# Kernel optimization log

Hardware: AMD Instinct MI355X
Metric: run time of the kernel (lower is better)

The kernel has to match this reference:

```python
import jax, jax.numpy as jnp
import numpy as np
import math

D_MODEL = 1024
N_HEADS = 16
HEAD_DIM = D_MODEL // N_HEADS
N_LEVELS = 4
B = 8
MAX_LEN = 1024
LN_EPS = 1e-5


def setup_inputs() -> dict:
    key = jax.random.key(0)
    ks = jax.random.split(key, 6)
    lengths = np.array([1024, 768, 512, 896, 640, 1024, 576, 704], dtype=np.int32)
    N = int(lengths.sum())  # 6144
    batch_offsets = jnp.asarray(np.concatenate([[0], np.cumsum(lengths)]).astype(np.int32))
    x = jax.random.normal(ks[0], (N, D_MODEL), jnp.float32)
    levels = jax.random.randint(ks[1], (N, 1), 0, N_LEVELS).astype(jnp.float32)
    coords = jax.random.uniform(ks[2], (N, 2), jnp.float32) * 64.0
    positions = jnp.concatenate([levels, coords], axis=-1)  # [N, 3] = (level, y, x)
    ln_gamma = jnp.ones((D_MODEL,), jnp.float32)
    ln_beta = jnp.zeros((D_MODEL,), jnp.float32)
    w_qkv = jax.random.normal(ks[3], (D_MODEL, 3 * D_MODEL), jnp.float32) / math.sqrt(D_MODEL)
    w_out = jax.random.normal(ks[4], (D_MODEL, D_MODEL), jnp.float32) / math.sqrt(D_MODEL)
    # learned per-level, per-head rotary frequencies for 2 spatial coords
    base = 10.0 ** (-2.0 * np.arange(HEAD_DIM // 2) / HEAD_DIM)  # rope_theta = 10.0
    rope_freqs = (jnp.asarray(base, jnp.float32)[None, None, :, None]
                  * (1.0 + 0.1 * jax.random.normal(ks[5], (N_LEVELS, N_HEADS, HEAD_DIM // 2, 2), jnp.float32)))
    return {"x": x, "positions": positions, "batch_offsets": batch_offsets,
            "ln_gamma": ln_gamma, "ln_beta": ln_beta, "w_qkv": w_qkv,
            "w_out": w_out, "rope_freqs": rope_freqs}


def _layernorm(x, g, b):
    mu = jnp.mean(x, axis=-1, keepdims=True)
    var = jnp.mean(jnp.square(x - mu), axis=-1, keepdims=True)
    return (x - mu) * jax.lax.rsqrt(var + LN_EPS) * g + b


def _forward(x, positions, batch_offsets, ln_gamma, ln_beta, w_qkv, w_out, rope_freqs):
    N = x.shape[0]
    residual = x
    h = _layernorm(x, ln_gamma, ln_beta)
    q, k, v = jnp.split(h @ w_qkv, 3, axis=-1)  # each [N, D]

    # ragged -> padded batch layout
    tok = jnp.arange(N)
    batch_ids = jnp.searchsorted(batch_offsets[1:], tok, side='right')  # [N]
    pos_in_seq = tok - batch_offsets[batch_ids]                         # [N]
    lengths = batch_offsets[1:] - batch_offsets[:-1]                    # [B]
    valid = jnp.arange(MAX_LEN)[None, :] < lengths[:, None]             # [B, L]

    def pad(t, fill=0.0):
        out = jnp.full((B, MAX_LEN) + t.shape[1:], fill, t.dtype)
        return out.at[batch_ids, pos_in_seq].set(t)

    qp = pad(q).reshape(B, MAX_LEN, N_HEADS, HEAD_DIM)
    kp = pad(k).reshape(B, MAX_LEN, N_HEADS, HEAD_DIM)
    vp = pad(v).reshape(B, MAX_LEN, N_HEADS, HEAD_DIM)
    posp = pad(positions, fill=1.0)  # padded positions filled with ones (as in torch code)

    # multilevel RoPE: per-level learned freqs over 2 spatial coords
    lvl = jnp.clip(posp[..., 0].astype(jnp.int32), 0, N_LEVELS - 1)  # [B, L]
    f = rope_freqs[lvl]                                              # [B, L, H, K, 2]
    ang = jnp.einsum('blhkc,blc->blhk', f, posp[..., 1:])            # [B, L, H, K]
    cos, sin = jnp.cos(ang), jnp.sin(ang)

    def rot(t):  # rotate consecutive pairs of head_dim
        t = t.reshape(B, MAX_LEN, N_HEADS, HEAD_DIM // 2, 2)
        a, b = t[..., 0], t[..., 1]
        return jnp.stack([a * cos - b * sin, a * sin + b * cos], axis=-1).reshape(
            B, MAX_LEN, N_HEADS, HEAD_DIM)

    qr, kr = rot(qp), rot(kp)

    # masked SDPA (padded keys excluded; padded query rows are dropped on un-pad)
    scale = 1.0 / math.sqrt(HEAD_DIM)
    scores = jnp.einsum('blhd,bmhd->bhlm', qr, kr) * scale
    scores = jnp.where(valid[:, None, None, :], scores, jnp.float32(-1e9))
    attn = jax.nn.softmax(scores, axis=-1)
    o = jnp.einsum('bhlm,bmhd->blhd', attn, vp).reshape(B, MAX_LEN, D_MODEL)

    o = o[batch_ids, pos_in_seq]  # back to packed [N, D]
    return o @ w_out + residual


def reference(x, positions, batch_offsets, ln_gamma, ln_beta, w_qkv, w_out, rope_freqs):
    return _forward(x, positions, batch_offsets, ln_gamma, ln_beta, w_qkv, w_out, rope_freqs)
```

## Files before the change

kernel.cpp:

```cpp
#include <hip/hip_runtime.h>


typedef float  f32x4  __attribute__((ext_vector_type(4)));
typedef __bf16 bf16x8 __attribute__((ext_vector_type(8)));
typedef __bf16 bf16x4 __attribute__((ext_vector_type(4)));
typedef short  s16x4  __attribute__((ext_vector_type(4)));
typedef short  s16x8  __attribute__((ext_vector_type(8)));
typedef unsigned short u16x4 __attribute__((ext_vector_type(4)));

typedef __attribute__((address_space(1))) void as1_void_t;
typedef __attribute__((address_space(3))) void as3_void_t;

static __device__ __forceinline__ unsigned short f2bf(float f) {
  unsigned int u = __float_as_uint(f);
  u += 0x7fffu + ((u >> 16) & 1u);
  return (unsigned short)(u >> 16);
}
static __device__ __forceinline__ float bf2f(unsigned short s) {
  return __uint_as_float(((unsigned int)s) << 16);
}

static __device__ __forceinline__ void gload_lds16(const void* g, void* l) {
  __builtin_amdgcn_global_load_lds((as1_void_t*)g, (as3_void_t*)l, 16, 0, 0);
}

static __device__ __forceinline__ f32x4 mfma32(bf16x8 a, bf16x8 b, f32x4 c) {
  return __builtin_amdgcn_mfma_f32_16x16x32_bf16(a, b, c, 0, 0, 0);
}
static __device__ __forceinline__ f32x4 mfma16(s16x4 a, s16x4 b, f32x4 c) {
  return __builtin_amdgcn_mfma_f32_16x16x16bf16_1k(a, b, c, 0, 0, 0);
}

__global__ __launch_bounds__(256) void ln_kernel(
    const float* __restrict__ x, const float* __restrict__ gamma,
    const float* __restrict__ beta, unsigned short* __restrict__ h, int Ntok) {
  int row  = blockIdx.x * 4 + (threadIdx.x >> 6);
  int lane = threadIdx.x & 63;
  const float* xr = x + (size_t)row * 1024;
  f32x4 v[4];
  float s = 0.f, ss = 0.f;
#pragma unroll
  for (int c = 0; c < 4; ++c) {
    v[c] = *(const f32x4*)(xr + c * 256 + lane * 4);
#pragma unroll
    for (int j = 0; j < 4; ++j) { s += v[c][j]; ss += v[c][j] * v[c][j]; }
  }
#pragma unroll
  for (int d = 1; d < 64; d <<= 1) {
    s  += __shfl_xor(s, d);
    ss += __shfl_xor(ss, d);
  }
  float mu  = s * (1.f / 1024.f);
  float var = ss * (1.f / 1024.f) - mu * mu;
  float inv = rsqrtf(var + 1e-5f);
#pragma unroll
  for (int c = 0; c < 4; ++c) {
    f32x4 gv = *(const f32x4*)(gamma + c * 256 + lane * 4);
    f32x4 bv = *(const f32x4*)(beta  + c * 256 + lane * 4);
    u16x4 hv;
#pragma unroll
    for (int j = 0; j < 4; ++j) hv[j] = f2bf((v[c][j] - mu) * inv * gv[j] + bv[j]);
    *(u16x4*)(h + (size_t)row * 1024 + c * 256 + lane * 4) = hv;
  }
}

__global__ __launch_bounds__(256) void transpose_bf16(
    const float* __restrict__ in, unsigned short* __restrict__ out, int R, int C) {
  __shared__ unsigned short tile[64][65];
  int c0 = blockIdx.x * 64, r0 = blockIdx.y * 64;
  int t = threadIdx.x;
  int tr = t >> 6, tc = t & 63;
#pragma unroll
  for (int i = 0; i < 16; ++i) {
    int rr = i * 4 + tr;
    tile[tc][rr] = f2bf(in[(size_t)(r0 + rr) * C + c0 + tc]);
  }
  __syncthreads();
#pragma unroll
  for (int i = 0; i < 16; ++i) {
    int cc = i * 4 + tr;
    out[(size_t)(c0 + cc) * R + r0 + tc] = tile[cc][tc];
  }
}

__global__ __launch_bounds__(256) void gemm_qkv(
    const unsigned short* __restrict__ A, const unsigned short* __restrict__ Bt,
    unsigned short* __restrict__ Cqkv, int M, int K) {
  __shared__ unsigned short Alds[128 * 32];
  __shared__ unsigned short Blds[128 * 32];
  int n0 = blockIdx.x * 128, m0 = blockIdx.y * 128;
  int t = threadIdx.x, lane = t & 63, wave = t >> 6;
  int wr = wave >> 1, wc = wave & 1;
  int r = lane & 15, g = lane >> 4;
  f32x4 acc[4][4] = {};

  int srow = lane >> 2;
  int scol = (lane & 3) * 8;

  for (int k0 = 0; k0 < K; k0 += 32) {
    __syncthreads();
#pragma unroll
    for (int c = 0; c < 2; ++c) {
      int seg = wave * 2 + c;
      gload_lds16(A  + (size_t)(m0 + seg * 16 + srow) * K + k0 + scol,
                  Alds + seg * 16 * 32);
      gload_lds16(Bt + (size_t)(n0 + seg * 16 + srow) * K + k0 + scol,
                  Blds + seg * 16 * 32);
    }
    __syncthreads();
    bf16x8 a[4], b[4];
#pragma unroll
    for (int m = 0; m < 4; ++m)
      a[m] = *(const bf16x8*)(Alds + (wr * 64 + m * 16 + r) * 32 + g * 8);
#pragma unroll
    for (int n = 0; n < 4; ++n)
      b[n] = *(const bf16x8*)(Blds + (wc * 64 + n * 16 + r) * 32 + g * 8);
#pragma unroll
    for (int m = 0; m < 4; ++m)
#pragma unroll
      for (int n = 0; n < 4; ++n)
        acc[m][n] = mfma32(a[m], b[n], acc[m][n]);
  }

#pragma unroll
  for (int mi = 0; mi < 4; ++mi) {
    int grow0 = m0 + wr * 64 + mi * 16 + g * 4;
#pragma unroll
    for (int ni = 0; ni < 4; ++ni) {
      int gcol = n0 + wc * 64 + ni * 16 + r;
      f32x4 v = acc[mi][ni];
#pragma unroll
      for (int e = 0; e < 4; ++e) {
        int which = gcol >> 10, rem = gcol & 1023, hh = rem >> 6, d = rem & 63;
        Cqkv[((size_t)(which * 16 + hh) * M + grow0 + e) * 64 + d] = f2bf(v[e]);
      }
    }
  }
}

__global__ __launch_bounds__(256) void gemm_n64(
    const unsigned short* __restrict__ A, const unsigned short* __restrict__ Bt,
    const float* __restrict__ residual, float* __restrict__ Cf,
    int M, int Ncols, int K) {
  __shared__ unsigned short Alds[128 * 32];
  __shared__ unsigned short Blds[64 * 32];
  int n0 = blockIdx.x * 64, m0 = blockIdx.y * 128;
  int t = threadIdx.x, lane = t & 63, wave = t >> 6;
  int wr = wave >> 1, wc = wave & 1;
  int r = lane & 15, g = lane >> 4;
  f32x4 acc[4][2] = {};

  int srow = lane >> 2;
  int scol = (lane & 3) * 8;

  for (int k0 = 0; k0 < K; k0 += 32) {
    __syncthreads();
#pragma unroll
    for (int c = 0; c < 2; ++c) {
      int seg = wave * 2 + c;
      gload_lds16(A + (size_t)(m0 + seg * 16 + srow) * K + k0 + scol,
                  Alds + seg * 16 * 32);
    }
    gload_lds16(Bt + (size_t)(n0 + wave * 16 + srow) * K + k0 + scol,
                Blds + wave * 16 * 32);
    __syncthreads();
    bf16x8 a[4], b[2];
#pragma unroll
    for (int m = 0; m < 4; ++m)
      a[m] = *(const bf16x8*)(Alds + (wr * 64 + m * 16 + r) * 32 + g * 8);
#pragma unroll
    for (int n = 0; n < 2; ++n)
      b[n] = *(const bf16x8*)(Blds + (wc * 32 + n * 16 + r) * 32 + g * 8);
#pragma unroll
    for (int m = 0; m < 4; ++m)
#pragma unroll
      for (int n = 0; n < 2; ++n)
        acc[m][n] = mfma32(a[m], b[n], acc[m][n]);
  }

#pragma unroll
  for (int mi = 0; mi < 4; ++mi) {
    int grow0 = m0 + wr * 64 + mi * 16 + g * 4;
#pragma unroll
    for (int ni = 0; ni < 2; ++ni) {
      int gcol = n0 + wc * 32 + ni * 16 + r;
      f32x4 v = acc[mi][ni];
#pragma unroll
      for (int e = 0; e < 4; ++e)
        Cf[(size_t)(grow0 + e) * Ncols + gcol] =
            v[e] + residual[(size_t)(grow0 + e) * Ncols + gcol];
    }
  }
}

__global__ __launch_bounds__(256) void rope_kernel(
    unsigned short* __restrict__ QKV, const float* __restrict__ pos,
    const float* __restrict__ freqs, int Ntok) {
  int t = blockIdx.x * 256 + threadIdx.x;
  if (t >= Ntok * 512) return;
  int kk = t & 31, h = (t >> 5) & 15, i = t >> 9;
  float lvlf = pos[i * 3 + 0];
  float py   = pos[i * 3 + 1];
  float px   = pos[i * 3 + 2];
  int lvl = (int)lvlf;
  lvl = lvl < 0 ? 0 : (lvl > 3 ? 3 : lvl);
  const float* fp = freqs + (((lvl * 16 + h) * 32 + kk) << 1);
  float ang = fp[0] * py + fp[1] * px;
  float s, c;
  __sincosf(ang, &s, &c);
  size_t qoff = ((size_t)h * Ntok + i) * 64 + 2 * kk;
  size_t koff = qoff + (size_t)16 * Ntok * 64;
  unsigned int q2 = *(const unsigned int*)(QKV + qoff);
  float qa = bf2f((unsigned short)(q2 & 0xffff));
  float qb = bf2f((unsigned short)(q2 >> 16));
  *(unsigned int*)(QKV + qoff) =
      (unsigned int)f2bf(qa * c - qb * s) | ((unsigned int)f2bf(qa * s + qb * c) << 16);
  unsigned int k2 = *(const unsigned int*)(QKV + koff);
  float ka = bf2f((unsigned short)(k2 & 0xffff));
  float kb = bf2f((unsigned short)(k2 >> 16));
  *(unsigned int*)(QKV + koff) =
      (unsigned int)f2bf(ka * c - kb * s) | ((unsigned int)f2bf(ka * s + kb * c) << 16);
}

__global__ __launch_bounds__(256) void vtrans_kernel(
    const unsigned short* __restrict__ Vp, unsigned short* __restrict__ VtG,
    int Ntok) {
  __shared__ unsigned short tile[64][72];
  int blk = blockIdx.x;
  int h = blk & 15, t0 = (blk >> 4) * 64;
  int t = threadIdx.x;
  {
    int tok = t >> 2, dc = (t & 3) * 16;
    const unsigned short* src = Vp + ((size_t)h * Ntok + t0 + tok) * 64 + dc;
    *(s16x8*)&tile[tok][dc]     = *(const s16x8*)src;
    *(s16x8*)&tile[tok][dc + 8] = *(const s16x8*)(src + 8);
  }
  __syncthreads();
  {
    int d = t >> 2, tc = (t & 3) * 16;
    s16x8 o0, o1;
#pragma unroll
    for (int j = 0; j < 8; ++j) {
      o0[j] = (short)tile[tc + j][d];
      o1[j] = (short)tile[tc + 8 + j][d];
    }
    unsigned short* dst = VtG + (size_t)(h * 64 + d) * Ntok + t0 + tc;
    *(s16x8*)dst       = o0;
    *(s16x8*)(dst + 8) = o1;
  }
}

__global__ __launch_bounds__(128, 3) void attn_kernel(
    const unsigned short* __restrict__ QKV,
    const unsigned short* __restrict__ VtG, const int* __restrict__ boff,
    unsigned short* __restrict__ O, int Ntok, int Bn) {
  __shared__ unsigned short Klds[64][72];
  __shared__ unsigned short Vt[64][72];
  const float SCALE_LOG2 = 0.125f * 1.44269504088896340736f;
  const s16x4 ones16 = {(short)0x3F80, (short)0x3F80, (short)0x3F80, (short)0x3F80};

  int bid = blockIdx.x;
  int nqb = Ntok >> 6;
  int qpx = nqb >> 3;
  int x = bid & 7, k = bid >> 3;
  int g = (k % qpx) * 8 + x;
  int h = k / qpx;
  int gt = g << 6;
  int b = 0;
#pragma unroll
  for (int j = 1; j < 8; ++j)
    if (j < Bn && boff[j] <= gt) b = j;
  int off = boff[b], len = boff[b + 1] - off;
  int q0 = gt - off;

  int t = threadIdx.x, lane = t & 63, wave = t >> 6;
  int r = lane & 15, g4 = lane >> 4;
  const unsigned short* Qg = QKV + (size_t)h * Ntok * 64;
  const unsigned short* Kg = QKV + (size_t)(16 + h) * Ntok * 64;
  int qmax = off + len - 1;

  bf16x8 qf[2][2];
#pragma unroll
  for (int qi = 0; qi < 2; ++qi) {
    int qtok = off + q0 + wave * 32 + qi * 16 + r;
    if (qtok > qmax) qtok = qmax;
#pragma unroll
    for (int c = 0; c < 2; ++c)
      qf[qi][c] = *(const bf16x8*)(Qg + (size_t)qtok * 64 + c * 32 + g4 * 8);
  }

  float m[2] = {-1e30f, -1e30f};
  f32x4 o[2][4] = {};
  f32x4 o_sum[2] = {};

  int srow = t >> 1, sseg = t & 1;
  const unsigned short* Vrow = VtG + (size_t)(h * 64 + srow) * Ntok;

  s16x8 kr[4], vr[4];
  {
    int ktok = off + srow; if (ktok > qmax) ktok = qmax;
#pragma unroll
    for (int c = 0; c < 4; ++c)
      kr[c] = *(const s16x8*)(Kg + (size_t)ktok * 64 + sseg * 32 + c * 8);
#pragma unroll
    for (int c = 0; c < 4; ++c) {
      int tc = sseg * 32 + c * 8; if (tc + 8 > len) tc = len - 8;
      vr[c] = *(const s16x8*)(Vrow + off + tc);
    }
  }

  for (int kt = 0; kt < len; kt += 64) {
    asm volatile("s_waitcnt lgkmcnt(0)" ::: "memory");
    __builtin_amdgcn_s_barrier();
    __builtin_amdgcn_sched_barrier(0);
#pragma unroll
    for (int c = 0; c < 4; ++c) {
      *(s16x8*)&Klds[srow][sseg * 32 + c * 8] = kr[c];
      *(s16x8*)&Vt[srow][sseg * 32 + c * 8]   = vr[c];
    }
    int ktn = kt + 64;
    if (ktn < len) {
      int ktok = off + ktn + srow; if (ktok > qmax) ktok = qmax;
#pragma unroll
      for (int c = 0; c < 4; ++c)
        kr[c] = *(const s16x8*)(Kg + (size_t)ktok * 64 + sseg * 32 + c * 8);
#pragma unroll
      for (int c = 0; c < 4; ++c) {
        int tc = ktn + sseg * 32 + c * 8; if (tc + 8 > len) tc = len - 8;
        vr[c] = *(const s16x8*)(Vrow + off + tc);
      }
    }
    asm volatile("s_waitcnt lgkmcnt(0)" ::: "memory");
    __builtin_amdgcn_s_barrier();
    __builtin_amdgcn_sched_barrier(0);

    f32x4 s[2][4];
    __builtin_amdgcn_s_setprio(1);
#pragma unroll
    for (int sub = 0; sub < 4; ++sub) {
      bf16x8 ka0 = *(const bf16x8*)(&Klds[sub * 16 + r][g4 * 8]);
      bf16x8 ka1 = *(const bf16x8*)(&Klds[sub * 16 + r][32 + g4 * 8]);
#pragma unroll
      for (int qi = 0; qi < 2; ++qi) {
        f32x4 acc = {};
        acc = mfma32(ka0, qf[qi][0], acc);
        acc = mfma32(ka1, qf[qi][1], acc);
        s[qi][sub] = acc;
      }
    }
    __builtin_amdgcn_s_setprio(0);

    bool tail = (kt + 64 > len);
    s16x4 pf[2][4];
#pragma unroll
    for (int qi = 0; qi < 2; ++qi) {
      float sc[4][4];
      float ms[4];
#pragma unroll
      for (int sub = 0; sub < 4; ++sub) {
#pragma unroll
        for (int e = 0; e < 4; ++e) {
          float v = s[qi][sub][e];
          if (tail && (kt + sub * 16 + 4 * g4 + e >= len)) v = -1e30f;
          sc[sub][e] = v;
        }
        ms[sub] = fmaxf(fmaxf(sc[sub][0], sc[sub][1]),
                        fmaxf(sc[sub][2], sc[sub][3]));
      }
      float tmax = fmaxf(fmaxf(ms[0], ms[1]), fmaxf(ms[2], ms[3]));
      float mq = m[qi];
      if (!__all(tmax * SCALE_LOG2 <= mq + 8.f)) {
        float tm = tmax * SCALE_LOG2;
        tm = fmaxf(tm, __shfl_xor(tm, 16));
        tm = fmaxf(tm, __shfl_xor(tm, 32));
        float mnew = fmaxf(mq, tm);
        float alpha = exp2f(mq - mnew);
        m[qi] = mnew; mq = mnew;
#pragma unroll
        for (int e = 0; e < 4; ++e) o_sum[qi][e] *= alpha;
#pragma unroll
        for (int dt = 0; dt < 4; ++dt)
#pragma unroll
          for (int e = 0; e < 4; ++e) o[qi][dt][e] *= alpha;
      }
#pragma unroll
      for (int sub = 0; sub < 4; ++sub) {
        bf16x4 pb;
#pragma unroll
        for (int e = 0; e < 4; ++e)
          pb[e] = (__bf16)exp2f(fmaf(sc[sub][e], SCALE_LOG2, -mq));
        pf[qi][sub] = __builtin_bit_cast(s16x4, pb);
      }
    }

    __builtin_amdgcn_s_setprio(1);
#pragma unroll
    for (int sub = 0; sub < 4; ++sub) {
      o_sum[0] = mfma16(pf[0][sub], ones16, o_sum[0]);
      o_sum[1] = mfma16(pf[1][sub], ones16, o_sum[1]);
    }
#pragma unroll
    for (int dt = 0; dt < 4; ++dt)
#pragma unroll
      for (int sub = 0; sub < 4; ++sub) {
        s16x4 vf = *(const s16x4*)(&Vt[dt * 16 + r][sub * 16 + 4 * g4]);
#pragma unroll
        for (int qi = 0; qi < 2; ++qi)
          o[qi][dt] = mfma16(pf[qi][sub], vf, o[qi][dt]);
      }
    __builtin_amdgcn_s_setprio(0);
  }

#pragma unroll
  for (int qi = 0; qi < 2; ++qi) {
    float il[4];
#pragma unroll
    for (int e = 0; e < 4; ++e) il[e] = 1.0f / o_sum[qi][e];
#pragma unroll
    for (int dt = 0; dt < 4; ++dt)
#pragma unroll
      for (int e = 0; e < 4; ++e) {
        int tl = q0 + wave * 32 + qi * 16 + 4 * g4 + e;
        if (tl < len)
          O[(size_t)(off + tl) * 1024 + h * 64 + dt * 16 + r] =
              f2bf(o[qi][dt][e] * il[e]);
      }
  }
}

extern "C" void kernel_launch(void* const* d_in, const int* in_sizes, int n_in,
                              void* d_out, int out_size, void* d_ws, size_t ws_size,
                              hipStream_t stream) {
  const float* x     = (const float*)d_in[0];
  const float* pos   = (const float*)d_in[1];
  const int*   boff  = (const int*)d_in[2];
  const float* gamma = (const float*)d_in[3];
  const float* beta  = (const float*)d_in[4];
  const float* wqkv  = (const float*)d_in[5];
  const float* wout  = (const float*)d_in[6];
  const float* freqs = (const float*)d_in[7];
  float* out = (float*)d_out;
  int N  = in_sizes[0] / 1024;
  int Bn = in_sizes[2] - 1;

  char* ws = (char*)d_ws;
  unsigned short* wqkvT = (unsigned short*)ws;
  unsigned short* woutT = (unsigned short*)(ws + (size_t)3072 * 1024 * 2);
  unsigned short* QKV   = (unsigned short*)(ws + (size_t)3072 * 1024 * 2 +
                                            (size_t)1024 * 1024 * 2);
  size_t qkvBytes = (size_t)48 * N * 64 * 2;
  unsigned short* hbuf = (unsigned short*)((char*)QKV + qkvBytes);
  unsigned short* VtG  = hbuf;
  unsigned short* Vp   = QKV + (size_t)32 * N * 64;
  unsigned short* Obuf = Vp;

  ln_kernel<<<N / 4, 256, 0, stream>>>(x, gamma, beta, hbuf, N);
  transpose_bf16<<<dim3(3072 / 64, 1024 / 64), 256, 0, stream>>>(wqkv, wqkvT, 1024, 3072);
  transpose_bf16<<<dim3(1024 / 64, 1024 / 64), 256, 0, stream>>>(wout, woutT, 1024, 1024);
  gemm_qkv<<<dim3(3072 / 128, N / 128), 256, 0, stream>>>(
      hbuf, wqkvT, QKV, N, 1024);
  rope_kernel<<<(N * 512) / 256, 256, 0, stream>>>(QKV, pos, freqs, N);
  vtrans_kernel<<<16 * (N / 64), 256, 0, stream>>>(Vp, VtG, N);
  attn_kernel<<<16 * (N / 64), 128, 0, stream>>>(QKV, VtG, boff, Obuf, N, Bn);
  gemm_n64<<<dim3(1024 / 64, N / 128), 256, 0, stream>>>(
      Obuf, woutT, x, out, N, 1024, 1024);
}
```

Before: 194.2 us.

## Use single-wave attention blocks reading K/V directly and widen output GEMM tile

The attention kernel now runs one 64-thread wave per block over 32 queries and drops the shared-memory K/V staging and barriers. Each wave loads K and transposed V fragments straight from global memory, relying on cache. A new block-to-(batch, head, query-window) mapping interleaves heads across blocks. Separately, the output projection GEMM widens its N tile from 64 to 128 to reuse A-tile loads. The trade is fewer barriers and more small blocks against more redundant global/L2 traffic per wave and fewer output-GEMM blocks.

```diff
diff --git a/kernel.cpp b/kernel.cpp
--- a/kernel.cpp
+++ b/kernel.cpp
@@ -138,17 +138,17 @@
   }
 }
 
-__global__ __launch_bounds__(256) void gemm_n64(
+__global__ __launch_bounds__(256) void gemm_out(
     const unsigned short* __restrict__ A, const unsigned short* __restrict__ Bt,
     const float* __restrict__ residual, float* __restrict__ Cf,
     int M, int Ncols, int K) {
   __shared__ unsigned short Alds[128 * 32];
-  __shared__ unsigned short Blds[64 * 32];
-  int n0 = blockIdx.x * 64, m0 = blockIdx.y * 128;
+  __shared__ unsigned short Blds[128 * 32];
+  int n0 = blockIdx.x * 128, m0 = blockIdx.y * 128;
   int t = threadIdx.x, lane = t & 63, wave = t >> 6;
   int wr = wave >> 1, wc = wave & 1;
   int r = lane & 15, g = lane >> 4;
-  f32x4 acc[4][2] = {};
+  f32x4 acc[4][4] = {};
 
   int srow = lane >> 2;
   int scol = (lane & 3) * 8;
@@ -158,23 +158,23 @@
 #pragma unroll
     for (int c = 0; c < 2; ++c) {
       int seg = wave * 2 + c;
-      gload_lds16(A + (size_t)(m0 + seg * 16 + srow) * K + k0 + scol,
+      gload_lds16(A  + (size_t)(m0 + seg * 16 + srow) * K + k0 + scol,
                   Alds + seg * 16 * 32);
-    }
-    gload_lds16(Bt + (size_t)(n0 + wave * 16 + srow) * K + k0 + scol,
-                Blds + wave * 16 * 32);
+      gload_lds16(Bt + (size_t)(n0 + seg * 16 + srow) * K + k0 + scol,
+                  Blds + seg * 16 * 32);
+    }
     __syncthreads();
-    bf16x8 a[4], b[2];
+    bf16x8 a[4], b[4];
 #pragma unroll
     for (int m = 0; m < 4; ++m)
       a[m] = *(const bf16x8*)(Alds + (wr * 64 + m * 16 + r) * 32 + g * 8);
 #pragma unroll
-    for (int n = 0; n < 2; ++n)
-      b[n] = *(const bf16x8*)(Blds + (wc * 32 + n * 16 + r) * 32 + g * 8);
+    for (int n = 0; n < 4; ++n)
+      b[n] = *(const bf16x8*)(Blds + (wc * 64 + n * 16 + r) * 32 + g * 8);
 #pragma unroll
     for (int m = 0; m < 4; ++m)
 #pragma unroll
-      for (int n = 0; n < 2; ++n)
+      for (int n = 0; n < 4; ++n)
         acc[m][n] = mfma32(a[m], b[n], acc[m][n]);
   }
 
@@ -182,8 +182,8 @@
   for (int mi = 0; mi < 4; ++mi) {
     int grow0 = m0 + wr * 64 + mi * 16 + g * 4;
 #pragma unroll
-    for (int ni = 0; ni < 2; ++ni) {
-      int gcol = n0 + wc * 32 + ni * 16 + r;
+    for (int ni = 0; ni < 4; ++ni) {
+      int gcol = n0 + wc * 64 + ni * 16 + r;
       f32x4 v = acc[mi][ni];
 #pragma unroll
       for (int e = 0; e < 4; ++e)
@@ -250,30 +250,31 @@
   }
 }
 
-__global__ __launch_bounds__(128, 3) void attn_kernel(
+__global__ __launch_bounds__(64, 3) void attn_kernel(
     const unsigned short* __restrict__ QKV,
     const unsigned short* __restrict__ VtG, const int* __restrict__ boff,
-    unsigned short* __restrict__ O, int Ntok, int Bn) {
-  __shared__ unsigned short Klds[64][72];
-  __shared__ unsigned short Vt[64][72];
+    unsigned short* __restrict__ O, int Ntok) {
   const float SCALE_LOG2 = 0.125f * 1.44269504088896340736f;
   const s16x4 ones16 = {(short)0x3F80, (short)0x3F80, (short)0x3F80, (short)0x3F80};
 
   int bid = blockIdx.x;
-  int nqb = Ntok >> 6;
-  int qpx = nqb >> 3;
-  int x = bid & 7, k = bid >> 3;
-  int g = (k % qpx) * 8 + x;
-  int h = k / qpx;
-  int gt = g << 6;
-  int b = 0;
-#pragma unroll
-  for (int j = 1; j < 8; ++j)
-    if (j < Bn && boff[j] <= gt) b = j;
+  int x = bid & 7, i = bid >> 3;
+  int b = 0, h = 0, qw = 0;
+  {
+    int cum = 0;
+#pragma unroll
+    for (int k = 0; k < 16; ++k) {
+      int p = x + 8 * k;
+      int bb = p >> 4;
+      int wc = (boff[bb + 1] - boff[bb]) >> 5;
+      if (i >= cum && i < cum + wc) { b = bb; h = p & 15; qw = i - cum; }
+      cum += wc;
+    }
+  }
   int off = boff[b], len = boff[b + 1] - off;
-  int q0 = gt - off;
-
-  int t = threadIdx.x, lane = t & 63, wave = t >> 6;
+  int q0 = qw * 32;
+
+  int lane = threadIdx.x & 63;
   int r = lane & 15, g4 = lane >> 4;
   const unsigned short* Qg = QKV + (size_t)h * Ntok * 64;
   const unsigned short* Kg = QKV + (size_t)(16 + h) * Ntok * 64;
@@ -282,7 +283,7 @@
   bf16x8 qf[2][2];
 #pragma unroll
   for (int qi = 0; qi < 2; ++qi) {
-    int qtok = off + q0 + wave * 32 + qi * 16 + r;
+    int qtok = off + q0 + qi * 16 + r;
     if (qtok > qmax) qtok = qmax;
 #pragma unroll
     for (int c = 0; c < 2; ++c)
@@ -293,53 +294,15 @@
   f32x4 o[2][4] = {};
   f32x4 o_sum[2] = {};
 
-  int srow = t >> 1, sseg = t & 1;
-  const unsigned short* Vrow = VtG + (size_t)(h * 64 + srow) * Ntok;
-
-  s16x8 kr[4], vr[4];
-  {
-    int ktok = off + srow; if (ktok > qmax) ktok = qmax;
-#pragma unroll
-    for (int c = 0; c < 4; ++c)
-      kr[c] = *(const s16x8*)(Kg + (size_t)ktok * 64 + sseg * 32 + c * 8);
-#pragma unroll
-    for (int c = 0; c < 4; ++c) {
-      int tc = sseg * 32 + c * 8; if (tc + 8 > len) tc = len - 8;
-      vr[c] = *(const s16x8*)(Vrow + off + tc);
-    }
-  }
-
   for (int kt = 0; kt < len; kt += 64) {
-    asm volatile("s_waitcnt lgkmcnt(0)" ::: "memory");
-    __builtin_amdgcn_s_barrier();
-    __builtin_amdgcn_sched_barrier(0);
-#pragma unroll
-    for (int c = 0; c < 4; ++c) {
-      *(s16x8*)&Klds[srow][sseg * 32 + c * 8] = kr[c];
-      *(s16x8*)&Vt[srow][sseg * 32 + c * 8]   = vr[c];
-    }
-    int ktn = kt + 64;
-    if (ktn < len) {
-      int ktok = off + ktn + srow; if (ktok > qmax) ktok = qmax;
-#pragma unroll
-      for (int c = 0; c < 4; ++c)
-        kr[c] = *(const s16x8*)(Kg + (size_t)ktok * 64 + sseg * 32 + c * 8);
-#pragma unroll
-      for (int c = 0; c < 4; ++c) {
-        int tc = ktn + sseg * 32 + c * 8; if (tc + 8 > len) tc = len - 8;
-        vr[c] = *(const s16x8*)(Vrow + off + tc);
-      }
-    }
-    asm volatile("s_waitcnt lgkmcnt(0)" ::: "memory");
-    __builtin_amdgcn_s_barrier();
-    __builtin_amdgcn_sched_barrier(0);
-
     f32x4 s[2][4];
     __builtin_amdgcn_s_setprio(1);
 #pragma unroll
     for (int sub = 0; sub < 4; ++sub) {
-      bf16x8 ka0 = *(const bf16x8*)(&Klds[sub * 16 + r][g4 * 8]);
-      bf16x8 ka1 = *(const bf16x8*)(&Klds[sub * 16 + r][32 + g4 * 8]);
+      int ktok = off + kt + sub * 16 + r;
+      if (ktok > qmax) ktok = qmax;
+      bf16x8 ka0 = *(const bf16x8*)(Kg + (size_t)ktok * 64 + g4 * 8);
+      bf16x8 ka1 = *(const bf16x8*)(Kg + (size_t)ktok * 64 + 32 + g4 * 8);
 #pragma unroll
       for (int qi = 0; qi < 2; ++qi) {
         f32x4 acc = {};
@@ -400,14 +363,18 @@
       o_sum[1] = mfma16(pf[1][sub], ones16, o_sum[1]);
     }
 #pragma unroll
-    for (int dt = 0; dt < 4; ++dt)
+    for (int dt = 0; dt < 4; ++dt) {
+      const unsigned short* vrow = VtG + (size_t)(h * 64 + dt * 16 + r) * Ntok;
 #pragma unroll
       for (int sub = 0; sub < 4; ++sub) {
-        s16x4 vf = *(const s16x4*)(&Vt[dt * 16 + r][sub * 16 + 4 * g4]);
+        int kk0 = kt + sub * 16 + 4 * g4;
+        if (kk0 + 4 > len) kk0 = len - 4;
+        s16x4 vf = *(const s16x4*)(vrow + off + kk0);
 #pragma unroll
         for (int qi = 0; qi < 2; ++qi)
           o[qi][dt] = mfma16(pf[qi][sub], vf, o[qi][dt]);
       }
+    }
     __builtin_amdgcn_s_setprio(0);
   }
 
@@ -420,7 +387,7 @@
     for (int dt = 0; dt < 4; ++dt)
 #pragma unroll
       for (int e = 0; e < 4; ++e) {
-        int tl = q0 + wave * 32 + qi * 16 + 4 * g4 + e;
+        int tl = q0 + qi * 16 + 4 * g4 + e;
         if (tl < len)
           O[(size_t)(off + tl) * 1024 + h * 64 + dt * 16 + r] =
               f2bf(o[qi][dt][e] * il[e]);
@@ -461,7 +428,7 @@
       hbuf, wqkvT, QKV, N, 1024);
   rope_kernel<<<(N * 512) / 256, 256, 0, stream>>>(QKV, pos, freqs, N);
   vtrans_kernel<<<16 * (N / 64), 256, 0, stream>>>(Vp, VtG, N);
-  attn_kernel<<<16 * (N / 64), 128, 0, stream>>>(QKV, VtG, boff, Obuf, N, Bn);
-  gemm_n64<<<dim3(1024 / 64, N / 128), 256, 0, stream>>>(
+  attn_kernel<<<16 * (N / 32), 64, 0, stream>>>(QKV, VtG, boff, Obuf, N);
+  gemm_out<<<dim3(1024 / 128, N / 128), 256, 0, stream>>>(
       Obuf, woutT, x, out, N, 1024, 1024);
 }
```

Measured after the change: 237.5 us. 1.22x slower.
